# Optimization experiments

Measured on AMD Instinct MI355X. Metric: run time of the kernel, lower is better.

## Reference

```python
import jax, jax.numpy as jnp
import numpy as np

N_BINS = 15


def setup_inputs() -> dict:
    key = jax.random.key(0)
    k1, k2 = jax.random.split(key)
    # [N, C] logits; scaled so confidences spread across bins
    logits = jax.random.normal(k1, (131072, 1000), dtype=jnp.float32) * 2.0
    target = jax.random.randint(k2, (131072,), 0, 1000, dtype=jnp.int64)
    return {"logits": logits, "target": target}


def reference(logits, target):
    # softmax + max/argmax over classes
    probs = jax.nn.softmax(logits, axis=-1)
    confidences = jnp.max(probs, axis=-1)            # [N]
    predictions = jnp.argmax(probs, axis=-1)         # [N]
    accuracies = (predictions == target).astype(jnp.float32)  # [N]

    # bin boundaries are linspace(0,1,n_bins+1); membership is (lower, upper],
    # equivalent to bin = ceil(conf * n_bins) - 1 clipped to [0, n_bins-1]
    bin_ids = jnp.clip(
        jnp.ceil(confidences * N_BINS).astype(jnp.int32) - 1, 0, N_BINS - 1
    )

    counts = jax.ops.segment_sum(jnp.ones_like(confidences), bin_ids, num_segments=N_BINS)
    sum_conf = jax.ops.segment_sum(confidences, bin_ids, num_segments=N_BINS)
    sum_acc = jax.ops.segment_sum(accuracies, bin_ids, num_segments=N_BINS)

    n = confidences.shape[0]
    prop_in_bin = counts / n
    safe_counts = jnp.maximum(counts, 1.0)
    avg_conf_in_bin = sum_conf / safe_counts
    acc_in_bin = sum_acc / safe_counts
    # NOTE: original code has NO abs() around the gap — kept faithful
    per_bin = (avg_conf_in_bin - acc_in_bin) * prop_in_bin
    ece = jnp.sum(jnp.where(counts > 0, per_bin, 0.0), keepdims=True)  # shape [1]

    return (ece, confidences.mean(), accuracies.mean())
```

## Files before the change

kernel.cpp:

```cpp
#include <hip/hip_runtime.h>
#include <hip/hip_bf16.h>
#include <math.h>


constexpr int N_CLASSES = 1000;
constexpr int NBINS     = 15;
constexpr int BLOCK     = 256;
constexpr int GRID      = 2048;
constexpr int WS_FLOATS = 3 * NBINS + 2;

__global__ __launch_bounds__(BLOCK) void ece_rows(const float* __restrict__ logits,
                                                  const int*   __restrict__ target,
                                                  float*       __restrict__ ws,
                                                  int nrows) {
    __shared__ float sacc[WS_FLOATS];
    const int t = threadIdx.x;
    if (t < WS_FLOATS) sacc[t] = 0.0f;
    __syncthreads();

    const int lane            = t & 63;
    const int wave            = t >> 6;
    const int waves_per_block = BLOCK / 64;
    const int gw              = blockIdx.x * waves_per_block + wave;
    const int nwaves          = gridDim.x * waves_per_block;

    for (int r = gw; r < nrows; r += nwaves) {
        const float4* rowp = reinterpret_cast<const float4*>(logits + (size_t)r * N_CLASSES);

        float m = -INFINITY;
        float s = 0.0f;
        int   idx = 0;

        #pragma unroll
        for (int c = 0; c < 4; ++c) {
            const int e0 = c * 256 + lane * 4;
            if (e0 < N_CLASSES) {
                float4 v = rowp[c * 64 + lane];
                float xs[4] = {v.x, v.y, v.z, v.w};
                #pragma unroll
                for (int j = 0; j < 4; ++j) {
                    float x = xs[j];
                    if (x > m) { s = s * __expf(m - x) + 1.0f; m = x; idx = e0 + j; }
                    else       { s += __expf(x - m); }
                }
            }
        }

        #pragma unroll
        for (int off = 32; off > 0; off >>= 1) {
            float m2 = __shfl_xor(m, off);
            float s2 = __shfl_xor(s, off);
            int   i2 = __shfl_xor(idx, off);
            float M  = fmaxf(m, m2);
            s = s * __expf(m - M) + s2 * __expf(m2 - M);
            if (m2 > m || (m2 == m && i2 < idx)) idx = i2;
            m = M;
        }

        if (lane == 0) {
            float conf = 1.0f / s;
            float acc  = (idx == target[r]) ? 1.0f : 0.0f;
            int bin = (int)ceilf(conf * (float)NBINS) - 1;
            bin = bin < 0 ? 0 : (bin > NBINS - 1 ? NBINS - 1 : bin);
            atomicAdd(&sacc[bin],             1.0f);
            atomicAdd(&sacc[NBINS + bin],     conf);
            atomicAdd(&sacc[2 * NBINS + bin], acc);
            atomicAdd(&sacc[3 * NBINS],       conf);
            atomicAdd(&sacc[3 * NBINS + 1],   acc);
        }
    }

    __syncthreads();
    if (t < WS_FLOATS) atomicAdd(&ws[t], sacc[t]);
}

__global__ void ece_finalize(const float* __restrict__ ws,
                             float*       __restrict__ out,
                             float inv_n) {
    const int t = threadIdx.x;
    float per = 0.0f;
    if (t < NBINS) {
        float c  = ws[t];
        float sc = ws[NBINS + t];
        float sa = ws[2 * NBINS + t];
        if (c > 0.0f) {
            float safe = fmaxf(c, 1.0f);
            per = (sc / safe - sa / safe) * (c * inv_n);
        }
    }
    #pragma unroll
    for (int off = 32; off > 0; off >>= 1) per += __shfl_xor(per, off);
    if (t == 0) {
        out[0] = per;
        out[1] = ws[3 * NBINS]     * inv_n;
        out[2] = ws[3 * NBINS + 1] * inv_n;
    }
}

extern "C" void kernel_launch(void* const* d_in, const int* in_sizes, int n_in,
                              void* d_out, int out_size, void* d_ws, size_t ws_size,
                              hipStream_t stream) {
    const float* logits = (const float*)d_in[0];
    const int*   target = (const int*)d_in[1];
    float*       ws     = (float*)d_ws;
    float*       out    = (float*)d_out;
    const int nrows = in_sizes[1];

    hipMemsetAsync(ws, 0, WS_FLOATS * sizeof(float), stream);
    ece_rows<<<GRID, BLOCK, 0, stream>>>(logits, target, ws, nrows);
    ece_finalize<<<1, 64, 0, stream>>>(ws, out, 1.0f / (float)nrows);
}
```

Before: 682.7 us.

## Prefetch next row, use two-pass max-then-sum softmax, and batch-load targets

Each wave now software-pipelines its rows by loading the next row's logits into registers while it processes the current one. The online softmax with a data-dependent branch is replaced by a two-pass approach: a max reduction across the wave first, then a branch-free exp-sum with a min-index argmax. Per-row target loads are replaced by one coalesced load per lane at kernel start, shuffled out as needed. These changes aim to hide memory latency and remove divergent branches and extra exps in the shuffle reduction, at the cost of more registers and an extra cross-lane reduction per row. The target preload assumes each wave handles at most 64 rows.

Measured after the change: 667.8 us. 2.2% less time.

```diff
diff --git a/kernel.cpp b/kernel.cpp
--- a/kernel.cpp
+++ b/kernel.cpp
@@ -18,48 +18,75 @@
     if (t < WS_FLOATS) sacc[t] = 0.0f;
     __syncthreads();
 
-    const int lane            = t & 63;
-    const int wave            = t >> 6;
-    const int waves_per_block = BLOCK / 64;
-    const int gw              = blockIdx.x * waves_per_block + wave;
-    const int nwaves          = gridDim.x * waves_per_block;
+    const int lane   = t & 63;
+    const int wave   = t >> 6;
+    const int gw     = blockIdx.x * (BLOCK / 64) + wave;
+    const int nwaves = gridDim.x * (BLOCK / 64);
 
-    for (int r = gw; r < nrows; r += nwaves) {
-        const float4* rowp = reinterpret_cast<const float4*>(logits + (size_t)r * N_CLASSES);
+    const int rk     = gw + lane * nwaves;
+    const int my_tgt = (rk < nrows) ? target[rk] : -1;
 
-        float m = -INFINITY;
-        float s = 0.0f;
-        int   idx = 0;
+    int c3 = 192 + lane;
+    if (c3 > 249) c3 = 249;
 
+    if (gw >= nrows) { __syncthreads(); if (t < WS_FLOATS) atomicAdd(&ws[t], sacc[t]); return; }
+
+    const float4* rowp = reinterpret_cast<const float4*>(logits + (size_t)gw * N_CLASSES);
+    float4 cur0 = rowp[lane];
+    float4 cur1 = rowp[64 + lane];
+    float4 cur2 = rowp[128 + lane];
+    float4 cur3 = rowp[c3];
+
+    int k = 0;
+    for (int r = gw; r < nrows; r += nwaves, ++k) {
+        float4 nxt0, nxt1, nxt2, nxt3;
+        const int rn = r + nwaves;
+        const bool have_next = rn < nrows;
+        if (have_next) {
+            const float4* np = reinterpret_cast<const float4*>(logits + (size_t)rn * N_CLASSES);
+            nxt0 = np[lane];
+            nxt1 = np[64 + lane];
+            nxt2 = np[128 + lane];
+            nxt3 = np[c3];
+        }
+
+        float xs[16];
+        xs[0]  = cur0.x; xs[1]  = cur0.y; xs[2]  = cur0.z; xs[3]  = cur0.w;
+        xs[4]  = cur1.x; xs[5]  = cur1.y; xs[6]  = cur1.z; xs[7]  = cur1.w;
+        xs[8]  = cur2.x; xs[9]  = cur2.y; xs[10] = cur2.z; xs[11] = cur2.w;
+        xs[12] = cur3.x; xs[13] = cur3.y; xs[14] = cur3.z; xs[15] = cur3.w;
+        if (lane >= 58) { xs[12] = xs[13] = xs[14] = xs[15] = -INFINITY; }
+
+        float m = xs[0];
+        #pragma unroll
+        for (int j = 1; j < 16; ++j) m = fmaxf(m, xs[j]);
+        #pragma unroll
+        for (int off = 32; off > 0; off >>= 1) m = fmaxf(m, __shfl_xor(m, off));
+
+        float s   = 0.0f;
+        int   idx = 0x7fffffff;
         #pragma unroll
         for (int c = 0; c < 4; ++c) {
-            const int e0 = c * 256 + lane * 4;
-            if (e0 < N_CLASSES) {
-                float4 v = rowp[c * 64 + lane];
-                float xs[4] = {v.x, v.y, v.z, v.w};
-                #pragma unroll
-                for (int j = 0; j < 4; ++j) {
-                    float x = xs[j];
-                    if (x > m) { s = s * __expf(m - x) + 1.0f; m = x; idx = e0 + j; }
-                    else       { s += __expf(x - m); }
-                }
+            #pragma unroll
+            for (int j = 0; j < 4; ++j) {
+                const int   q = c * 4 + j;
+                const float x = xs[q];
+                s += __expf(x - m);
+                const int e = c * 256 + lane * 4 + j;
+                if (x == m && e < idx) idx = e;
             }
         }
-
         #pragma unroll
         for (int off = 32; off > 0; off >>= 1) {
-            float m2 = __shfl_xor(m, off);
-            float s2 = __shfl_xor(s, off);
-            int   i2 = __shfl_xor(idx, off);
-            float M  = fmaxf(m, m2);
-            s = s * __expf(m - M) + s2 * __expf(m2 - M);
-            if (m2 > m || (m2 == m && i2 < idx)) idx = i2;
-            m = M;
+            s  += __shfl_xor(s, off);
+            idx = min(idx, __shfl_xor(idx, off));
         }
 
+        const int tr = __shfl(my_tgt, k);
+
         if (lane == 0) {
-            float conf = 1.0f / s;
-            float acc  = (idx == target[r]) ? 1.0f : 0.0f;
+            const float conf = 1.0f / s;
+            const float acc  = (idx == tr) ? 1.0f : 0.0f;
             int bin = (int)ceilf(conf * (float)NBINS) - 1;
             bin = bin < 0 ? 0 : (bin > NBINS - 1 ? NBINS - 1 : bin);
             atomicAdd(&sacc[bin],             1.0f);
@@ -68,6 +95,8 @@
             atomicAdd(&sacc[3 * NBINS],       conf);
             atomicAdd(&sacc[3 * NBINS + 1],   acc);
         }
+
+        if (have_next) { cur0 = nxt0; cur1 = nxt1; cur2 = nxt2; cur3 = nxt3; }
     }
 
     __syncthreads();
```
